# Optimization experiments

Hardware: AMD Instinct MI355X
Metric: run time of the kernel (lower is better)

Reference implementation:

```python
import jax, jax.numpy as jnp
import numpy as np

D_MODEL = 1024
D_STATE = 16
D_CONV = 4
EXPAND = 2
D_INNER = EXPAND * D_MODEL          # 2048
DT_RANK = (D_MODEL + 15) // 16      # 64
B_SZ, SEQ = 2, 1024
LN_EPS = 1e-6


def setup_inputs() -> dict:
    key = jax.random.key(0)
    ks = jax.random.split(key, 12)
    s = 0.02
    x = jax.random.normal(ks[0], (B_SZ, SEQ, D_MODEL), dtype=jnp.float32)
    W_in = jax.random.normal(ks[1], (D_MODEL, 2 * D_INNER), dtype=jnp.float32) * s
    conv_w = jax.random.normal(ks[2], (D_INNER, D_CONV), dtype=jnp.float32) * s
    conv_b = jnp.zeros((D_INNER,), dtype=jnp.float32)
    W_xproj = jax.random.normal(ks[3], (D_INNER, DT_RANK + 2 * D_STATE), dtype=jnp.float32) * s
    W_dt = jax.random.normal(ks[4], (DT_RANK, D_INNER), dtype=jnp.float32) * (DT_RANK ** -0.5)
    # dt bias ~ log-uniform init as in Mamba (softplus^-1 of dt in [1e-3, 1e-1])
    dt = jnp.exp(jax.random.uniform(ks[5], (D_INNER,)) * (np.log(0.1) - np.log(1e-3)) + np.log(1e-3))
    b_dt = dt + jnp.log(-jnp.expm1(-dt))  # inverse softplus
    A_log = jnp.log(jnp.broadcast_to(jnp.arange(1, D_STATE + 1, dtype=jnp.float32), (D_INNER, D_STATE)))
    D_param = jnp.ones((D_INNER,), dtype=jnp.float32)
    W_out = jax.random.normal(ks[6], (D_INNER, D_MODEL), dtype=jnp.float32) * s
    gamma = jnp.ones((D_MODEL,), dtype=jnp.float32)
    beta = jnp.zeros((D_MODEL,), dtype=jnp.float32)
    return {"x": x, "W_in": W_in, "conv_w": conv_w, "conv_b": conv_b,
            "W_xproj": W_xproj, "W_dt": W_dt, "b_dt": b_dt, "A_log": A_log,
            "D_param": D_param, "W_out": W_out, "gamma": gamma, "beta": beta}


def _mamba(x, W_in, conv_w, conv_b, W_xproj, W_dt, b_dt, A_log, D_param, W_out):
    B, L, _ = x.shape
    xz = x @ W_in                                  # [B,L,2*d_inner]
    xi, z = jnp.split(xz, 2, axis=-1)              # [B,L,d_inner] each
    # causal depthwise conv1d, kernel D_CONV
    xp = jnp.pad(xi, ((0, 0), (D_CONV - 1, 0), (0, 0)))
    xc = conv_b
    for k in range(D_CONV):
        xc = xc + xp[:, k:k + L, :] * conv_w[:, k]
    xc = jax.nn.silu(xc)                           # [B,L,d_inner]
    x_dbl = xc @ W_xproj                           # [B,L,dt_rank+2*d_state]
    dt_r = x_dbl[..., :DT_RANK]
    B_ssm = x_dbl[..., DT_RANK:DT_RANK + D_STATE]  # [B,L,d_state]
    C_ssm = x_dbl[..., DT_RANK + D_STATE:]         # [B,L,d_state]
    dt = jax.nn.softplus(dt_r @ W_dt + b_dt)       # [B,L,d_inner]
    A = -jnp.exp(A_log)                            # [d_inner,d_state]
    dA = jnp.exp(dt[..., None] * A)                # [B,L,d_inner,d_state]
    dBu = dt[..., None] * B_ssm[:, :, None, :] * xc[..., None]
    # selective scan over time (time-major for lax.scan)
    dA_t = jnp.moveaxis(dA, 1, 0)                  # [L,B,d_inner,d_state]
    dBu_t = jnp.moveaxis(dBu, 1, 0)
    C_t = jnp.moveaxis(C_ssm, 1, 0)                # [L,B,d_state]
    h0 = jnp.zeros((B, D_INNER, D_STATE), dtype=x.dtype)

    def step(h, inp):
        a, bu, c = inp
        h = a * h + bu
        y = jnp.einsum('bdn,bn->bd', h, c)
        return h, y

    _, ys = jax.lax.scan(step, h0, (dA_t, dBu_t, C_t))
    y = jnp.moveaxis(ys, 0, 1)                     # [B,L,d_inner]
    y = y + xc * D_param
    y = y * jax.nn.silu(z)
    return y @ W_out                               # [B,L,d_model]


def reference(x, W_in, conv_w, conv_b, W_xproj, W_dt, b_dt, A_log, D_param, W_out, gamma, beta):
    m = _mamba(x, W_in, conv_w, conv_b, W_xproj, W_dt, b_dt, A_log, D_param, W_out)
    mu = jnp.mean(m, axis=-1, keepdims=True)
    var = jnp.mean(jnp.square(m - mu), axis=-1, keepdims=True)
    ln = (m - mu) * jax.lax.rsqrt(var + LN_EPS) * gamma + beta
    return x + ln
```

## Files before the change

kernel.cpp:

```cpp
#include <hip/hip_runtime.h>
#include <math.h>

#define DM   1024
#define DI   2048
#define DS   16
#define DTR  64
#define NB   2
#define SEQL 1024
#define NTOK (NB*SEQL)
#define XND  96
#define XNP  128
#define CK   64
#define CL   16

typedef __bf16 bf16x8 __attribute__((ext_vector_type(8)));
typedef float  f32x4  __attribute__((ext_vector_type(4)));

#define PREP_BLOCKS 10624

__device__ inline void trans_tile(const float* __restrict__ W,
                                  __bf16* __restrict__ WT, int K, int N,
                                  int n0, int k0, int tid, __bf16 (*t)[33])
{
    const int tx = tid & 31, ty = tid >> 5;
    #pragma unroll
    for (int i = 0; i < 4; i++)
        t[ty * 4 + i][tx] = (__bf16)W[(size_t)(k0 + ty * 4 + i) * N + n0 + tx];
    __syncthreads();
    #pragma unroll
    for (int i = 0; i < 4; i++)
        WT[(size_t)(n0 + ty * 4 + i) * K + k0 + tx] = t[tx][ty * 4 + i];
}

__global__ __launch_bounds__(256) void prep(
    const float* __restrict__ x, const float* __restrict__ W_in,
    const float* __restrict__ W_out, const float* __restrict__ W_dt,
    const float* __restrict__ W_xprj,
    __bf16* __restrict__ xb, __bf16* __restrict__ W_inT,
    __bf16* __restrict__ W_outT, __bf16* __restrict__ WdtT,
    __bf16* __restrict__ W_xprT, float* __restrict__ xdbl,
    float* __restrict__ mbuf)
{
    __shared__ __bf16 t[32][33];
    int bid = blockIdx.x;
    const int tid = threadIdx.x;

    if (bid < 2304) {
        const int i = bid * 1024 + tid * 4;
        const float4 z = {0.f, 0.f, 0.f, 0.f};
        if (i < 262144) *reinterpret_cast<float4*>(&xdbl[i]) = z;
        else            *reinterpret_cast<float4*>(&mbuf[i - 262144]) = z;
        return;
    }
    bid -= 2304;
    if (bid < 1024) {
        const int e = (bid * 256 + tid) * 8;
        const float4 v0 = *reinterpret_cast<const float4*>(&x[e]);
        const float4 v1 = *reinterpret_cast<const float4*>(&x[e + 4]);
        bf16x8 o;
        o[0] = (__bf16)v0.x; o[1] = (__bf16)v0.y; o[2] = (__bf16)v0.z; o[3] = (__bf16)v0.w;
        o[4] = (__bf16)v1.x; o[5] = (__bf16)v1.y; o[6] = (__bf16)v1.z; o[7] = (__bf16)v1.w;
        *reinterpret_cast<bf16x8*>(&xb[e]) = o;
        return;
    }
    bid -= 1024;
    if (bid < 4096) {
        trans_tile(W_in, W_inT, DM, 2 * DI, (bid & 127) * 32, (bid >> 7) * 32, tid, t);
        return;
    }
    bid -= 4096;
    if (bid < 2048) {
        trans_tile(W_out, W_outT, DI, DM, (bid & 31) * 32, (bid >> 5) * 32, tid, t);
        return;
    }
    bid -= 2048;
    if (bid < 128) {
        trans_tile(W_dt, WdtT, DTR, DI, (bid & 63) * 32, (bid >> 6) * 32, tid, t);
        return;
    }
    bid -= 128;
    {
        const int idx = bid * 256 + tid;
        const int k = idx & (DI - 1);
        const int n = idx >> 11;
        W_xprT[(size_t)n * DI + k] = (n < XND) ? (__bf16)W_xprj[(size_t)k * XND + n]
                                               : (__bf16)0.f;
    }
}

template<int MODE, int SWZ>
__global__ __launch_bounds__(256) void gemm_bf16(
    const __bf16* __restrict__ A, const __bf16* __restrict__ Bt,
    void* __restrict__ Cp, int M, int N, int K, int ldc,
    const float* __restrict__ bias)
{
    __shared__ __bf16 As[2][128 * 64];
    __shared__ __bf16 Bs[2][128 * 64];
    const int tid  = threadIdx.x;
    const int lane = tid & 63;
    const int wid  = tid >> 6;
    const int wr   = wid >> 1, wc = wid & 1;

    int bx = blockIdx.x, by = blockIdx.y;
    if (SWZ != 0) {
        const int gx = gridDim.x, gy = gridDim.y;
        const int nxy = gx * gy;
        const int q = nxy >> 3;
        int lin = by * gx + bx;
        lin = (lin & 7) * q + (lin >> 3);
        if (SWZ == 1) { by = lin / gx; bx = lin % gx; }
        else          { bx = lin / gy; by = lin % gy; }
    }
    const int brow = by * 128, bcol = bx * 128;
    const int kper = K / gridDim.z;
    const int kbeg = blockIdx.z * kper, kend = kbeg + kper;

    f32x4 acc[4][4] = {};

    auto stage = [&](int buf, int k0) {
        if (MODE == 2) {
            const float* Af = reinterpret_cast<const float*>(A);
            #pragma unroll
            for (int p = 0; p < 4; p++) {
                const int i = p * 256 + tid;
                const int r = i >> 3;
                const int j = i & 7;
                const float4 v0 = *reinterpret_cast<const float4*>(
                    &Af[(size_t)(brow + r) * XNP + j * 8]);
                const float4 v1 = *reinterpret_cast<const float4*>(
                    &Af[(size_t)(brow + r) * XNP + j * 8 + 4]);
                bf16x8 o;
                o[0] = (__bf16)v0.x; o[1] = (__bf16)v0.y; o[2] = (__bf16)v0.z; o[3] = (__bf16)v0.w;
                o[4] = (__bf16)v1.x; o[5] = (__bf16)v1.y; o[6] = (__bf16)v1.z; o[7] = (__bf16)v1.w;
                *reinterpret_cast<bf16x8*>(&As[buf][r * 64 + ((j ^ (r & 7))) * 8]) = o;
            }
        } else {
            #pragma unroll
            for (int p = 0; p < 4; p++) {
                const int i = p * 256 + tid;
                const int r = i >> 3;
                const int gc = ((i & 7) ^ (r & 7)) * 8;
                __builtin_amdgcn_global_load_lds(
                    (const __attribute__((address_space(1))) void*)(A + (size_t)(brow + r) * K + k0 + gc),
                    (__attribute__((address_space(3))) void*)(&As[buf][i * 8]), 16, 0, 0);
            }
        }
        #pragma unroll
        for (int p = 0; p < 4; p++) {
            const int i = p * 256 + tid;
            const int r = i >> 3;
            const int gc = ((i & 7) ^ (r & 7)) * 8;
            __builtin_amdgcn_global_load_lds(
                (const __attribute__((address_space(1))) void*)(Bt + (size_t)(bcol + r) * K + k0 + gc),
                (__attribute__((address_space(3))) void*)(&Bs[buf][i * 8]), 16, 0, 0);
        }
    };

    const int nt = (kend - kbeg) >> 6;
    stage(0, kbeg);
    __syncthreads();
    int cur = 0;
    for (int t = 0; t < nt; t++) {
        if (t + 1 < nt) stage(cur ^ 1, kbeg + ((t + 1) << 6));
        const __bf16* Ab = &As[cur][0];
        const __bf16* Bb = &Bs[cur][0];
        bf16x8 a[2][4], b[2][4];
        const int rA = wr * 64 + (lane & 15);
        const int rB = wc * 64 + (lane & 15);
        const int cq = lane >> 4;
        const int rx = lane & 7;
        #pragma unroll
        for (int ks = 0; ks < 2; ks++) {
            const int sl = ((ks * 4 + cq) ^ rx) * 8;
            #pragma unroll
            for (int m = 0; m < 4; m++) {
                a[ks][m] = *reinterpret_cast<const bf16x8*>(&Ab[(rA + m * 16) * 64 + sl]);
                b[ks][m] = *reinterpret_cast<const bf16x8*>(&Bb[(rB + m * 16) * 64 + sl]);
            }
        }
        #pragma unroll
        for (int ks = 0; ks < 2; ks++)
            #pragma unroll
            for (int m = 0; m < 4; m++)
                #pragma unroll
                for (int n = 0; n < 4; n++)
                    acc[m][n] = __builtin_amdgcn_mfma_f32_16x16x32_bf16(
                        a[ks][m], b[ks][n], acc[m][n], 0, 0, 0);
        __syncthreads();
        cur ^= 1;
    }
    const int crow = brow + wr * 64 + (lane >> 4) * 4;
    const int ccol = bcol + wc * 64 + (lane & 15);
    #pragma unroll
    for (int m = 0; m < 4; m++)
        #pragma unroll
        for (int n = 0; n < 4; n++) {
            const int col = ccol + n * 16;
            #pragma unroll
            for (int j = 0; j < 4; j++) {
                const size_t idx = (size_t)(crow + m * 16 + j) * ldc + col;
                if (MODE == 0) {
                    ((float*)Cp)[idx] = acc[m][n][j];
                } else if (MODE == 1) {
                    atomicAdd(&((float*)Cp)[idx], acc[m][n][j]);
                } else if (MODE == 2) {
                    const float v = acc[m][n][j] + bias[col];
                    ((__bf16*)Cp)[idx] =
                        (__bf16)(fmaxf(v, 0.f) + log1pf(__expf(-fabsf(v))));
                } else {
                    ((__bf16*)Cp)[idx] = (__bf16)acc[m][n][j];
                }
            }
        }
}

__global__ __launch_bounds__(256) void conv_silu(
    const __bf16* __restrict__ xzb, const float* __restrict__ conv_w,
    const float* __restrict__ conv_b, __bf16* __restrict__ xcb)
{
    const int g  = blockIdx.x * 256 + threadIdx.x;
    const int d0 = (g & 255) * 8;
    const int tok = g >> 8;
    const int t   = tok & (SEQL - 1);

    float4 wv[8];
    #pragma unroll
    for (int j = 0; j < 8; j++)
        wv[j] = *reinterpret_cast<const float4*>(&conv_w[(d0 + j) * 4]);
    float acc[8];
    {
        const float4 b0 = *reinterpret_cast<const float4*>(&conv_b[d0]);
        const float4 b1 = *reinterpret_cast<const float4*>(&conv_b[d0 + 4]);
        acc[0] = b0.x; acc[1] = b0.y; acc[2] = b0.z; acc[3] = b0.w;
        acc[4] = b1.x; acc[5] = b1.y; acc[6] = b1.z; acc[7] = b1.w;
    }
    #pragma unroll
    for (int k = 0; k < 4; k++) {
        const int tt = t + k - 3;
        if (tt >= 0) {
            const bf16x8 v = *reinterpret_cast<const bf16x8*>(
                &xzb[(size_t)(tok + k - 3) * (2 * DI) + d0]);
            #pragma unroll
            for (int j = 0; j < 8; j++) {
                const float wk = (k == 0) ? wv[j].x : (k == 1) ? wv[j].y
                               : (k == 2) ? wv[j].z : wv[j].w;
                acc[j] += (float)v[j] * wk;
            }
        }
    }
    bf16x8 o;
    #pragma unroll
    for (int j = 0; j < 8; j++) {
        const float a = acc[j];
        o[j] = (__bf16)(a / (1.f + __expf(-a)));
    }
    *reinterpret_cast<bf16x8*>(&xcb[(size_t)g * 8]) = o;
}

__global__ __launch_bounds__(256) void scan_partial(
    const __bf16* __restrict__ xcb, const float* __restrict__ xdbl,
    const __bf16* __restrict__ dtb, const float* __restrict__ A_log,
    float* __restrict__ hpart, float* __restrict__ sdtb)
{
    __shared__ float Bsh[CL][16];
    const int tid = threadIdx.x;
    const int d = blockIdx.x * 256 + tid;
    const int c = blockIdx.y, b = blockIdx.z;
    const size_t base = (size_t)b * SEQL + c * CL;
    {
        const int st = tid >> 4, sg = tid & 15;
        Bsh[st][sg] = xdbl[(base + st) * XNP + DTR + sg];
    }
    float dtv[CL], xcv[CL];
    #pragma unroll
    for (int t = 0; t < CL; t++) {
        dtv[t] = (float)dtb[(base + t) * DI + d];
        xcv[t] = (float)xcb[(base + t) * DI + d];
    }
    float Av[16];
    #pragma unroll
    for (int i = 0; i < 4; i++) {
        const float4 v = *reinterpret_cast<const float4*>(&A_log[(size_t)d * 16 + i * 4]);
        Av[i*4+0] = -__expf(v.x); Av[i*4+1] = -__expf(v.y);
        Av[i*4+2] = -__expf(v.z); Av[i*4+3] = -__expf(v.w);
    }
    __syncthreads();
    float h[16] = {};
    float sdt = 0.f;
    #pragma unroll
    for (int t = 0; t < CL; t++) {
        sdt += dtv[t];
        const float dx = dtv[t] * xcv[t];
        #pragma unroll
        for (int n = 0; n < 16; n++)
            h[n] = __expf(dtv[t] * Av[n]) * h[n] + dx * Bsh[t][n];
    }
    const size_t ob = ((size_t)(b * CK + c) * DI + d) * 16;
    #pragma unroll
    for (int i = 0; i < 4; i++) {
        float4 v; v.x = h[i*4]; v.y = h[i*4+1]; v.z = h[i*4+2]; v.w = h[i*4+3];
        *reinterpret_cast<float4*>(&hpart[ob + i * 4]) = v;
    }
    sdtb[(size_t)(b * CK + c) * DI + d] = sdt;
}

__global__ __launch_bounds__(256) void scan_combine(
    const float* __restrict__ A_log, const float* __restrict__ sdtb,
    const float* __restrict__ hpart, float* __restrict__ hentry)
{
    const int idx = blockIdx.x * 256 + threadIdx.x;
    const int n = idx & 15;
    const int d = (idx >> 4) & (DI - 1);
    const int b = idx >> 15;
    const float A = -__expf(A_log[(size_t)d * 16 + n]);
    float h = 0.f;
    #pragma unroll
    for (int cb = 0; cb < CK / 16; cb++) {
        float hl[16], sv[16];
        #pragma unroll
        for (int j = 0; j < 16; j++) {
            const int c = cb * 16 + j;
            hl[j] = hpart[((size_t)(b * CK + c) * DI + d) * 16 + n];
            sv[j] = sdtb[(size_t)(b * CK + c) * DI + d];
        }
        #pragma unroll
        for (int j = 0; j < 16; j++) {
            const int c = cb * 16 + j;
            hentry[((size_t)(b * CK + c) * DI + d) * 16 + n] = h;
            h = __expf(A * sv[j]) * h + hl[j];
        }
    }
}

__global__ __launch_bounds__(256) void scan_final(
    const __bf16* __restrict__ xzb, const __bf16* __restrict__ xcb,
    const float* __restrict__ xdbl, const __bf16* __restrict__ dtb,
    const float* __restrict__ A_log, const float* __restrict__ Dp,
    const float* __restrict__ hentry, __bf16* __restrict__ yb)
{
    __shared__ float Bsh[CL][16];
    __shared__ float Csh[CL][16];
    const int tid = threadIdx.x;
    const int d = blockIdx.x * 256 + tid;
    const int c = blockIdx.y, b = blockIdx.z;
    const size_t base = (size_t)b * SEQL + c * CL;
    {
        const int st = tid >> 4, sg = tid & 15;
        Bsh[st][sg] = xdbl[(base + st) * XNP + DTR + sg];
        Csh[st][sg] = xdbl[(base + st) * XNP + DTR + DS + sg];
    }
    float dtv[CL], xcv[CL], zv[CL];
    #pragma unroll
    for (int t = 0; t < CL; t++) {
        dtv[t] = (float)dtb[(base + t) * DI + d];
        xcv[t] = (float)xcb[(base + t) * DI + d];
        zv[t]  = (float)xzb[(base + t) * (2 * DI) + DI + d];
    }
    float Av[16];
    #pragma unroll
    for (int i = 0; i < 4; i++) {
        const float4 v = *reinterpret_cast<const float4*>(&A_log[(size_t)d * 16 + i * 4]);
        Av[i*4+0] = -__expf(v.x); Av[i*4+1] = -__expf(v.y);
        Av[i*4+2] = -__expf(v.z); Av[i*4+3] = -__expf(v.w);
    }
    float h[16];
    const size_t ob = ((size_t)(b * CK + c) * DI + d) * 16;
    #pragma unroll
    for (int i = 0; i < 4; i++) {
        const float4 v = *reinterpret_cast<const float4*>(&hentry[ob + i * 4]);
        h[i*4] = v.x; h[i*4+1] = v.y; h[i*4+2] = v.z; h[i*4+3] = v.w;
    }
    const float Dv = Dp[d];
    __syncthreads();
    #pragma unroll
    for (int t = 0; t < CL; t++) {
        const float dx = dtv[t] * xcv[t];
        float y = 0.f;
        #pragma unroll
        for (int n = 0; n < 16; n++) {
            h[n] = __expf(dtv[t] * Av[n]) * h[n] + dx * Bsh[t][n];
            y += h[n] * Csh[t][n];
        }
        y += xcv[t] * Dv;
        y *= zv[t] / (1.f + __expf(-zv[t]));
        yb[(base + t) * DI + d] = (__bf16)y;
    }
}

__global__ __launch_bounds__(256) void ln_add(
    const float* __restrict__ x, const float* __restrict__ m,
    const float* __restrict__ gamma, const float* __restrict__ beta,
    float* __restrict__ out)
{
    const int tok = blockIdx.x;
    const int tid = threadIdx.x;
    const int lane = tid & 63, wave = tid >> 6;
    __shared__ float red[4];
    __shared__ float stats[2];

    const float4 v = reinterpret_cast<const float4*>(&m[(size_t)tok * DM])[tid];
    float s = v.x + v.y + v.z + v.w;
    #pragma unroll
    for (int o = 32; o > 0; o >>= 1) s += __shfl_down(s, o, 64);
    if (lane == 0) red[wave] = s;
    __syncthreads();
    if (tid == 0) stats[0] = (red[0] + red[1] + red[2] + red[3]) * (1.f / DM);
    __syncthreads();
    const float mu = stats[0];
    const float dx = v.x - mu, dy = v.y - mu, dz = v.z - mu, dw = v.w - mu;
    float q = dx * dx + dy * dy + dz * dz + dw * dw;
    #pragma unroll
    for (int o = 32; o > 0; o >>= 1) q += __shfl_down(q, o, 64);
    if (lane == 0) red[wave] = q;
    __syncthreads();
    if (tid == 0)
        stats[1] = rsqrtf((red[0] + red[1] + red[2] + red[3]) * (1.f / DM) + 1e-6f);
    __syncthreads();
    const float rs = stats[1];

    const float4 g  = reinterpret_cast<const float4*>(gamma)[tid];
    const float4 bb = reinterpret_cast<const float4*>(beta)[tid];
    const float4 xv = reinterpret_cast<const float4*>(&x[(size_t)tok * DM])[tid];
    float4 o;
    o.x = xv.x + dx * rs * g.x + bb.x;
    o.y = xv.y + dy * rs * g.y + bb.y;
    o.z = xv.z + dz * rs * g.z + bb.z;
    o.w = xv.w + dw * rs * g.w + bb.w;
    reinterpret_cast<float4*>(&out[(size_t)tok * DM])[tid] = o;
}

extern "C" void kernel_launch(void* const* d_in, const int* in_sizes, int n_in,
                              void* d_out, int out_size, void* d_ws, size_t ws_size,
                              hipStream_t stream)
{
    const float* x      = (const float*)d_in[0];
    const float* W_in   = (const float*)d_in[1];
    const float* conv_w = (const float*)d_in[2];
    const float* conv_b = (const float*)d_in[3];
    const float* W_xprj = (const float*)d_in[4];
    const float* W_dt   = (const float*)d_in[5];
    const float* b_dt   = (const float*)d_in[6];
    const float* A_log  = (const float*)d_in[7];
    const float* D_par  = (const float*)d_in[8];
    const float* W_out  = (const float*)d_in[9];
    const float* gamma  = (const float*)d_in[10];
    const float* beta   = (const float*)d_in[11];
    float* out = (float*)d_out;

    char* w = (char*)d_ws;
    __bf16* xzb    = (__bf16*)(w + 0);
    __bf16* xcb    = (__bf16*)(w + 16777216);
    float*  xdbl   = (float*) (w + 25165824);
    __bf16* dtb    = (__bf16*)(w + 26214400);
    float*  mbuf   = (float*) (w + 34603008);
    float*  hpart  = (float*) (w + 42991616);
    float*  sdtb   = (float*) (w + 59768832);
    __bf16* xb     = (__bf16*)(w + 60817408);
    __bf16* W_inT  = (__bf16*)(w + 65011712);
    __bf16* W_outT = (__bf16*)(w + 73400320);
    __bf16* W_xprT = (__bf16*)(w + 77594624);
    __bf16* WdtT   = (__bf16*)(w + 78118912);
    __bf16* yb     = (__bf16*)(w + 78381056);
    float*  hentry = (float*) (w + 86769664);

    prep<<<PREP_BLOCKS, 256, 0, stream>>>(
        x, W_in, W_out, W_dt, W_xprj, xb, W_inT, W_outT, WdtT, W_xprT, xdbl, mbuf);

    gemm_bf16<3, 2><<<dim3(32, 16, 1), 256, 0, stream>>>(
        xb, W_inT, xzb, NTOK, 2 * DI, DM, 2 * DI, nullptr);

    conv_silu<<<(NTOK * DI / 8) / 256, 256, 0, stream>>>(xzb, conv_w, conv_b, xcb);

    gemm_bf16<1, 0><<<dim3(1, 16, 16), 256, 0, stream>>>(
        xcb, W_xprT, xdbl, NTOK, XNP, DI, XNP, nullptr);

    gemm_bf16<2, 0><<<dim3(16, 16, 1), 256, 0, stream>>>(
        (const __bf16*)xdbl, WdtT, dtb, NTOK, DI, DTR, DI, b_dt);

    scan_partial<<<dim3(DI / 256, CK, NB), 256, 0, stream>>>(
        xcb, xdbl, dtb, A_log, hpart, sdtb);
    scan_combine<<<NB * DI * DS / 256, 256, 0, stream>>>(A_log, sdtb, hpart, hentry);
    scan_final<<<dim3(DI / 256, CK, NB), 256, 0, stream>>>(
        xzb, xcb, xdbl, dtb, A_log, D_par, hentry, yb);

    gemm_bf16<1, 1><<<dim3(8, 16, 4), 256, 0, stream>>>(
        yb, W_outT, mbuf, NTOK, DM, DI, DM, nullptr);

    ln_add<<<NTOK, 256, 0, stream>>>(x, mbuf, gamma, beta, out);
}
```

Baseline: 183.5 us.

## Replace atomic split-K output with bf16 partials, bf16 scan states, larger transpose tiles

The output GEMM now writes four bf16 split-K partial buffers instead of atomically adding into a zeroed fp32 buffer, and ln_add sums the partials. This removes the memset of the output buffer and the atomic traffic. The scan's chunk states (hpart, hentry) are stored in bf16 to halve that memory traffic, and weight transposes use 64x64 tiles with fewer blocks. In exchange, the partials and the carried scan states lose precision.

```diff
diff --git a/kernel.cpp b/kernel.cpp
--- a/kernel.cpp
+++ b/kernel.cpp
@@ -14,22 +14,23 @@
 #define CL   16
 
 typedef __bf16 bf16x8 __attribute__((ext_vector_type(8)));
+typedef __bf16 bf16x4 __attribute__((ext_vector_type(4)));
 typedef float  f32x4  __attribute__((ext_vector_type(4)));
 
-#define PREP_BLOCKS 10624
-
-__device__ inline void trans_tile(const float* __restrict__ W,
-                                  __bf16* __restrict__ WT, int K, int N,
-                                  int n0, int k0, int tid, __bf16 (*t)[33])
-{
-    const int tx = tid & 31, ty = tid >> 5;
-    #pragma unroll
-    for (int i = 0; i < 4; i++)
-        t[ty * 4 + i][tx] = (__bf16)W[(size_t)(k0 + ty * 4 + i) * N + n0 + tx];
-    __syncthreads();
-    #pragma unroll
-    for (int i = 0; i < 4; i++)
-        WT[(size_t)(n0 + ty * 4 + i) * K + k0 + tx] = t[tx][ty * 4 + i];
+#define PREP_BLOCKS 3872
+
+__device__ inline void trans_tile64(const float* __restrict__ W,
+                                    __bf16* __restrict__ WT, int K, int N,
+                                    int n0, int k0, int tid, __bf16 (*t)[65])
+{
+    const int tx = tid & 63, ty = tid >> 6;
+    #pragma unroll
+    for (int i = 0; i < 16; i++)
+        t[ty * 16 + i][tx] = (__bf16)W[(size_t)(k0 + ty * 16 + i) * N + n0 + tx];
+    __syncthreads();
+    #pragma unroll
+    for (int i = 0; i < 16; i++)
+        WT[(size_t)(n0 + ty * 16 + i) * K + k0 + tx] = t[tx][ty * 16 + i];
 }
 
 __global__ __launch_bounds__(256) void prep(
@@ -38,21 +39,19 @@
     const float* __restrict__ W_xprj,
     __bf16* __restrict__ xb, __bf16* __restrict__ W_inT,
     __bf16* __restrict__ W_outT, __bf16* __restrict__ WdtT,
-    __bf16* __restrict__ W_xprT, float* __restrict__ xdbl,
-    float* __restrict__ mbuf)
-{
-    __shared__ __bf16 t[32][33];
+    __bf16* __restrict__ W_xprT, float* __restrict__ xdbl)
+{
+    __shared__ __bf16 t[64][65];
     int bid = blockIdx.x;
     const int tid = threadIdx.x;
 
-    if (bid < 2304) {
+    if (bid < 256) {
         const int i = bid * 1024 + tid * 4;
         const float4 z = {0.f, 0.f, 0.f, 0.f};
-        if (i < 262144) *reinterpret_cast<float4*>(&xdbl[i]) = z;
-        else            *reinterpret_cast<float4*>(&mbuf[i - 262144]) = z;
+        *reinterpret_cast<float4*>(&xdbl[i]) = z;
         return;
     }
-    bid -= 2304;
+    bid -= 256;
     if (bid < 1024) {
         const int e = (bid * 256 + tid) * 8;
         const float4 v0 = *reinterpret_cast<const float4*>(&x[e]);
@@ -64,21 +63,21 @@
         return;
     }
     bid -= 1024;
-    if (bid < 4096) {
-        trans_tile(W_in, W_inT, DM, 2 * DI, (bid & 127) * 32, (bid >> 7) * 32, tid, t);
+    if (bid < 1024) {
+        trans_tile64(W_in, W_inT, DM, 2 * DI, (bid & 63) * 64, (bid >> 6) * 64, tid, t);
         return;
     }
-    bid -= 4096;
-    if (bid < 2048) {
-        trans_tile(W_out, W_outT, DI, DM, (bid & 31) * 32, (bid >> 5) * 32, tid, t);
+    bid -= 1024;
+    if (bid < 512) {
+        trans_tile64(W_out, W_outT, DI, DM, (bid & 15) * 64, (bid >> 4) * 64, tid, t);
         return;
     }
-    bid -= 2048;
-    if (bid < 128) {
-        trans_tile(W_dt, WdtT, DTR, DI, (bid & 63) * 32, (bid >> 6) * 32, tid, t);
+    bid -= 512;
+    if (bid < 32) {
+        trans_tile64(W_dt, WdtT, DTR, DI, bid * 64, 0, tid, t);
         return;
     }
-    bid -= 128;
+    bid -= 32;
     {
         const int idx = bid * 256 + tid;
         const int k = idx & (DI - 1);
@@ -191,6 +190,7 @@
     }
     const int crow = brow + wr * 64 + (lane >> 4) * 4;
     const int ccol = bcol + wc * 64 + (lane & 15);
+    __bf16* Cb3 = (__bf16*)Cp + (size_t)blockIdx.z * ((MODE == 3) ? (size_t)M * ldc : 0);
     #pragma unroll
     for (int m = 0; m < 4; m++)
         #pragma unroll
@@ -208,7 +208,7 @@
                     ((__bf16*)Cp)[idx] =
                         (__bf16)(fmaxf(v, 0.f) + log1pf(__expf(-fabsf(v))));
                 } else {
-                    ((__bf16*)Cp)[idx] = (__bf16)acc[m][n][j];
+                    Cb3[idx] = (__bf16)acc[m][n][j];
                 }
             }
         }
@@ -260,7 +260,7 @@
 __global__ __launch_bounds__(256) void scan_partial(
     const __bf16* __restrict__ xcb, const float* __restrict__ xdbl,
     const __bf16* __restrict__ dtb, const float* __restrict__ A_log,
-    float* __restrict__ hpart, float* __restrict__ sdtb)
+    __bf16* __restrict__ hpart, float* __restrict__ sdtb)
 {
     __shared__ float Bsh[CL][16];
     const int tid = threadIdx.x;
@@ -296,17 +296,17 @@
             h[n] = __expf(dtv[t] * Av[n]) * h[n] + dx * Bsh[t][n];
     }
     const size_t ob = ((size_t)(b * CK + c) * DI + d) * 16;
-    #pragma unroll
-    for (int i = 0; i < 4; i++) {
-        float4 v; v.x = h[i*4]; v.y = h[i*4+1]; v.z = h[i*4+2]; v.w = h[i*4+3];
-        *reinterpret_cast<float4*>(&hpart[ob + i * 4]) = v;
-    }
+    bf16x8 o0, o1;
+    #pragma unroll
+    for (int i = 0; i < 8; i++) { o0[i] = (__bf16)h[i]; o1[i] = (__bf16)h[i + 8]; }
+    *reinterpret_cast<bf16x8*>(&hpart[ob])     = o0;
+    *reinterpret_cast<bf16x8*>(&hpart[ob + 8]) = o1;
     sdtb[(size_t)(b * CK + c) * DI + d] = sdt;
 }
 
 __global__ __launch_bounds__(256) void scan_combine(
     const float* __restrict__ A_log, const float* __restrict__ sdtb,
-    const float* __restrict__ hpart, float* __restrict__ hentry)
+    const __bf16* __restrict__ hpart, __bf16* __restrict__ hentry)
 {
     const int idx = blockIdx.x * 256 + threadIdx.x;
     const int n = idx & 15;
@@ -320,13 +320,13 @@
         #pragma unroll
         for (int j = 0; j < 16; j++) {
             const int c = cb * 16 + j;
-            hl[j] = hpart[((size_t)(b * CK + c) * DI + d) * 16 + n];
+            hl[j] = (float)hpart[((size_t)(b * CK + c) * DI + d) * 16 + n];
             sv[j] = sdtb[(size_t)(b * CK + c) * DI + d];
         }
         #pragma unroll
         for (int j = 0; j < 16; j++) {
             const int c = cb * 16 + j;
-            hentry[((size_t)(b * CK + c) * DI + d) * 16 + n] = h;
+            hentry[((size_t)(b * CK + c) * DI + d) * 16 + n] = (__bf16)h;
             h = __expf(A * sv[j]) * h + hl[j];
         }
     }
@@ -336,7 +336,7 @@
     const __bf16* __restrict__ xzb, const __bf16* __restrict__ xcb,
     const float* __restrict__ xdbl, const __bf16* __restrict__ dtb,
     const float* __restrict__ A_log, const float* __restrict__ Dp,
-    const float* __restrict__ hentry, __bf16* __restrict__ yb)
+    const __bf16* __restrict__ hentry, __bf16* __restrict__ yb)
 {
     __shared__ float Bsh[CL][16];
     __shared__ float Csh[CL][16];
@@ -365,10 +365,11 @@
     }
     float h[16];
     const size_t ob = ((size_t)(b * CK + c) * DI + d) * 16;
-    #pragma unroll
-    for (int i = 0; i < 4; i++) {
-        const float4 v = *reinterpret_cast<const float4*>(&hentry[ob + i * 4]);
-        h[i*4] = v.x; h[i*4+1] = v.y; h[i*4+2] = v.z; h[i*4+3] = v.w;
+    {
+        const bf16x8 v0 = *reinterpret_cast<const bf16x8*>(&hentry[ob]);
+        const bf16x8 v1 = *reinterpret_cast<const bf16x8*>(&hentry[ob + 8]);
+        #pragma unroll
+        for (int i = 0; i < 8; i++) { h[i] = (float)v0[i]; h[i + 8] = (float)v1[i]; }
     }
     const float Dv = Dp[d];
     __syncthreads();
@@ -388,7 +389,7 @@
 }
 
 __global__ __launch_bounds__(256) void ln_add(
-    const float* __restrict__ x, const float* __restrict__ m,
+    const float* __restrict__ x, const __bf16* __restrict__ mpart,
     const float* __restrict__ gamma, const float* __restrict__ beta,
     float* __restrict__ out)
 {
@@ -398,7 +399,14 @@
     __shared__ float red[4];
     __shared__ float stats[2];
 
-    const float4 v = reinterpret_cast<const float4*>(&m[(size_t)tok * DM])[tid];
+    float4 v = {0.f, 0.f, 0.f, 0.f};
+    #pragma unroll
+    for (int p = 0; p < 4; p++) {
+        const bf16x4 mv = *reinterpret_cast<const bf16x4*>(
+            &mpart[((size_t)p * NTOK + tok) * DM + tid * 4]);
+        v.x += (float)mv[0]; v.y += (float)mv[1];
+        v.z += (float)mv[2]; v.w += (float)mv[3];
+    }
     float s = v.x + v.y + v.z + v.w;
     #pragma unroll
     for (int o = 32; o > 0; o >>= 1) s += __shfl_down(s, o, 64);
@@ -452,19 +460,19 @@
     __bf16* xcb    = (__bf16*)(w + 16777216);
     float*  xdbl   = (float*) (w + 25165824);
     __bf16* dtb    = (__bf16*)(w + 26214400);
-    float*  mbuf   = (float*) (w + 34603008);
-    float*  hpart  = (float*) (w + 42991616);
-    float*  sdtb   = (float*) (w + 59768832);
-    __bf16* xb     = (__bf16*)(w + 60817408);
-    __bf16* W_inT  = (__bf16*)(w + 65011712);
-    __bf16* W_outT = (__bf16*)(w + 73400320);
-    __bf16* W_xprT = (__bf16*)(w + 77594624);
-    __bf16* WdtT   = (__bf16*)(w + 78118912);
-    __bf16* yb     = (__bf16*)(w + 78381056);
-    float*  hentry = (float*) (w + 86769664);
+    __bf16* mpart  = (__bf16*)(w + 34603008);
+    __bf16* hpart  = (__bf16*)(w + 51380224);
+    __bf16* hentry = (__bf16*)(w + 59768832);
+    float*  sdtb   = (float*) (w + 68157440);
+    __bf16* xb     = (__bf16*)(w + 68681728);
+    __bf16* W_inT  = (__bf16*)(w + 72876032);
+    __bf16* W_outT = (__bf16*)(w + 81264640);
+    __bf16* W_xprT = (__bf16*)(w + 85458944);
+    __bf16* WdtT   = (__bf16*)(w + 85983232);
+    __bf16* yb     = (__bf16*)(w + 86245376);
 
     prep<<<PREP_BLOCKS, 256, 0, stream>>>(
-        x, W_in, W_out, W_dt, W_xprj, xb, W_inT, W_outT, WdtT, W_xprT, xdbl, mbuf);
+        x, W_in, W_out, W_dt, W_xprj, xb, W_inT, W_outT, WdtT, W_xprT, xdbl);
 
     gemm_bf16<3, 2><<<dim3(32, 16, 1), 256, 0, stream>>>(
         xb, W_inT, xzb, NTOK, 2 * DI, DM, 2 * DI, nullptr);
@@ -483,8 +491,8 @@
     scan_final<<<dim3(DI / 256, CK, NB), 256, 0, stream>>>(
         xzb, xcb, xdbl, dtb, A_log, D_par, hentry, yb);
 
-    gemm_bf16<1, 1><<<dim3(8, 16, 4), 256, 0, stream>>>(
-        yb, W_outT, mbuf, NTOK, DM, DI, DM, nullptr);
-
-    ln_add<<<NTOK, 256, 0, stream>>>(x, mbuf, gamma, beta, out);
-}
+    gemm_bf16<3, 1><<<dim3(8, 16, 4), 256, 0, stream>>>(
+        yb, W_outT, mpart, NTOK, DM, DI, DM, nullptr);
+
+    ln_add<<<NTOK, 256, 0, stream>>>(x, mpart, gamma, beta, out);
+}
```

Result: faster. 171.2 us (-6.7%).
